# Performance work log

Measured on AMD Instinct MI355X. Metric: run time of the kernel, lower is better.

## Reference

```python
import jax, jax.numpy as jnp
import numpy as np

B, C, H, W = 4, 256, 64, 64
D = C // 8  # qk projection dim = 32


def setup_inputs() -> dict:
    key = jax.random.key(0)
    ks = jax.random.split(key, 10)
    s = 1.0 / np.sqrt(C)
    return {
        "semantic_map": jax.random.normal(ks[0], (B, C, H, W), jnp.float32),
        "structural_map": jax.random.normal(ks[1], (B, C, H, W), jnp.float32),
        "Wq": jax.random.normal(ks[2], (D, C), jnp.float32) * s,
        "bq": jax.random.normal(ks[3], (D,), jnp.float32) * 0.01,
        "Wk": jax.random.normal(ks[4], (D, C), jnp.float32) * s,
        "bk": jax.random.normal(ks[5], (D,), jnp.float32) * 0.01,
        "Wv": jax.random.normal(ks[6], (C, C), jnp.float32) * s,
        "bv": jax.random.normal(ks[7], (C,), jnp.float32) * 0.01,
        "gamma": jnp.zeros((1,), jnp.float32) + 0.5,  # nonzero so the attention path matters
    }


def reference(semantic_map, structural_map, Wq, bq, Wk, bk, Wv, bv, gamma):
    b, c, h, w = semantic_map.shape
    n = h * w
    # 1x1 convs == per-pixel linear projections
    q = jnp.einsum("bchw,dc->bdhw", semantic_map, Wq) + bq[None, :, None, None]
    k = jnp.einsum("bchw,dc->bdhw", structural_map, Wk) + bk[None, :, None, None]
    v = jnp.einsum("bchw,oc->bohw", structural_map, Wv) + bv[None, :, None, None]
    q = q.reshape(b, -1, n).transpose(0, 2, 1)  # (B, HW, D)
    k = k.reshape(b, -1, n)                     # (B, D, HW)
    v = v.reshape(b, c, n)                      # (B, C, HW)
    energy = jnp.einsum("bid,bdj->bij", q, k)   # (B, HW, HW)
    attention = jax.nn.softmax(energy, axis=-1)
    # out[b,c,i] = sum_j v[b,c,j] * attention[b,i,j]
    out = jnp.einsum("bcj,bij->bci", v, attention).reshape(b, c, h, w)
    return gamma * out + semantic_map
```

## Files before the change

kernel.cpp:

```cpp
#include <hip/hip_runtime.h>

#define B_   4
#define C_   256
#define N_   4096
#define D_   32
#define CP   264

typedef _Float16 half8  __attribute__((ext_vector_type(8)));
typedef _Float16 half4v __attribute__((ext_vector_type(4)));
typedef _Float16 half2v __attribute__((ext_vector_type(2)));
typedef float    f32x4  __attribute__((ext_vector_type(4)));

__global__ __launch_bounds__(256) void wcvt_kernel(
    const float* __restrict__ Wq, const float* __restrict__ Wk,
    const float* __restrict__ Wv, _Float16* __restrict__ Wh)
{
    const int idx = blockIdx.x * 256 + threadIdx.x;
    const int kk  = idx & 31;
    const int row = (idx >> 5) & 15;
    const int kc  = (idx >> 9) & 7;
    const int t   = idx >> 12;
    const int c   = kc*32 + kk;
    float v;
    if (t < 2)      v = Wq[(t*16 + row)*C_ + c];
    else if (t < 4) v = Wk[((t-2)*16 + row)*C_ + c];
    else            v = Wv[((t-4)*16 + row)*C_ + c];
    Wh[idx] = (_Float16)v;
}

__global__ __launch_bounds__(512, 4) void proj_kernel(
    const float* __restrict__ sem, const float* __restrict__ str,
    const _Float16* __restrict__ Wh,
    const float* __restrict__ bq, const float* __restrict__ bk,
    const float* __restrict__ bv,
    _Float16* __restrict__ Qh, _Float16* __restrict__ Kh, _Float16* __restrict__ Vh2)
{
    __shared__ __align__(16) _Float16 smem[2 * 64 * CP];
    _Float16* s_x = smem;
    _Float16* s_s = smem + 64 * CP;

    const int bid = blockIdx.x;
    const int nt6 = bid & 63;
    const int b   = bid >> 6;
    const int n0  = nt6 * 64;
    const int tid = threadIdx.x;
    const int w    = tid >> 6;
    const int lane = tid & 63;
    const int quad = lane >> 4;
    const int l15  = lane & 15;

    const int cnt = (w < 4) ? 3 : 2;
    const int t0  = (w < 4) ? w*3 : 12 + (w-4)*2;

    f32x4 acc[3][4];
    #pragma unroll
    for (int i = 0; i < 3; ++i)
        #pragma unroll
        for (int j = 0; j < 4; ++j) { acc[i][j][0]=0.f; acc[i][j][1]=0.f; acc[i][j][2]=0.f; acc[i][j][3]=0.f; }

    const size_t xbase = (size_t)b * C_ * N_;

    #pragma unroll
    for (int r = 0; r < 4; ++r) {
        const int slot = r*512 + tid;
        const int nq = slot & 15;
        const int cp = slot >> 4;
        const float* p0 = str + xbase + (size_t)(2*cp) * N_ + n0 + nq*4;
        const float4 a4 = *(const float4*)p0;
        const float4 b4 = *(const float4*)(p0 + N_);
        #pragma unroll
        for (int t = 0; t < 4; ++t) {
            half2v hp; hp[0] = (_Float16)a4[t]; hp[1] = (_Float16)b4[t];
            *(half2v*)(s_x + (nq*4 + t)*CP + 2*cp) = hp;
        }
        const float* p1 = sem + xbase + (size_t)(2*cp) * N_ + n0 + nq*4;
        const float4 c4 = *(const float4*)p1;
        const float4 d4 = *(const float4*)(p1 + N_);
        #pragma unroll
        for (int t = 0; t < 4; ++t) {
            half2v hp; hp[0] = (_Float16)c4[t]; hp[1] = (_Float16)d4[t];
            *(half2v*)(s_s + (nq*4 + t)*CP + 2*cp) = hp;
        }
    }
    __syncthreads();

    auto afload = [&](half8 (&af)[3], int kc) {
        #pragma unroll
        for (int mi = 0; mi < 3; ++mi)
            if (mi < cnt)
                af[mi] = *(const half8*)(Wh + ((size_t)(((t0+mi)*8 + kc)*16 + l15))*32 + quad*8);
    };
    auto bload = [&](half8 (&bfr)[4], half8 (&sfr)[4], int kc) {
        #pragma unroll
        for (int nt = 0; nt < 4; ++nt)
            bfr[nt] = *(const half8*)(s_x + (nt*16 + l15)*CP + kc*32 + quad*8);
        if (w == 0) {
            #pragma unroll
            for (int nt = 0; nt < 4; ++nt)
                sfr[nt] = *(const half8*)(s_s + (nt*16 + l15)*CP + kc*32 + quad*8);
        }
    };
    auto domfma = [&](const half8 (&af)[3], const half8 (&bfr)[4], const half8 (&sfr)[4]) {
        #pragma unroll
        for (int mi = 0; mi < 3; ++mi) {
            if (mi >= cnt) break;
            const bool useS = (t0 + mi) < 2;
            #pragma unroll
            for (int nt = 0; nt < 4; ++nt)
                acc[mi][nt] = __builtin_amdgcn_mfma_f32_16x16x32_f16(
                                  af[mi], useS ? sfr[nt] : bfr[nt], acc[mi][nt], 0, 0, 0);
        }
    };

    half8 afA[3], afB[3];
    afload(afA, 0);
    #pragma unroll 1
    for (int kc2 = 0; kc2 < 4; ++kc2) {
        const int kc = kc2*2;
        half8 bfr[4], sfr[4];
        bload(bfr, sfr, kc);
        afload(afB, kc+1);
        domfma(afA, bfr, sfr);
        half8 bfr2[4], sfr2[4];
        bload(bfr2, sfr2, kc+1);
        if (kc2 < 3) afload(afA, kc+2);
        domfma(afB, bfr2, sfr2);
    }

    #pragma unroll
    for (int mi = 0; mi < 3; ++mi) {
        if (mi >= cnt) break;
        const int t = t0 + mi;
        if (t < 4) {
            const bool isq = (t < 2);
            const int  tt  = isq ? t : (t - 2);
            f32x4 b4 = *(const f32x4*)((isq ? bq : bk) + tt*16 + quad*4);
            _Float16* dst = isq ? Qh : Kh;
            const int dc  = tt*2 + (quad >> 1);
            const int off = (quad & 1) * 4;
            #pragma unroll
            for (int nt = 0; nt < 4; ++nt) {
                const int n = n0 + nt*16 + l15;
                f32x4 a = acc[mi][nt];
                half4v hq;
                hq[0]=(_Float16)(a[0]+b4[0]); hq[1]=(_Float16)(a[1]+b4[1]);
                hq[2]=(_Float16)(a[2]+b4[2]); hq[3]=(_Float16)(a[3]+b4[3]);
                *(half4v*)(dst + ((size_t)(b*4 + dc) * N_ + n) * 8 + off) = hq;
            }
        }
    }
    __syncthreads();

    #pragma unroll
    for (int mi = 0; mi < 3; ++mi) {
        if (mi >= cnt) break;
        const int t = t0 + mi;
        if (t >= 4) {
            const int ctg = t - 4;
            f32x4 b4 = *(const f32x4*)(bv + ctg*16 + quad*4);
            _Float16* sv = smem + (w*3 + mi)*1024;
            #pragma unroll
            for (int nt = 0; nt < 4; ++nt) {
                const int js = nt & 1;
                const int hb = nt >> 1;
                f32x4 a = acc[mi][nt];
                #pragma unroll
                for (int r = 0; r < 4; ++r)
                    sv[hb*512 + ((l15>>2)*16 + quad*4 + r)*8 + js*4 + (l15&3)]
                        = (_Float16)(a[r] + b4[r]);
            }
        }
    }
    {
        _Float16* vb = Vh2 + (size_t)b * (size_t)N_ * C_;
        const int jc2_0 = n0 >> 5;
        #pragma unroll
        for (int mi = 0; mi < 3; ++mi) {
            if (mi >= cnt) break;
            const int t = t0 + mi;
            if (t >= 4) {
                const int ctg = t - 4;
                const _Float16* sv = smem + (w*3 + mi)*1024;
                #pragma unroll
                for (int hb = 0; hb < 2; ++hb) {
                    half8 vv = *(const half8*)(&sv[hb*512 + lane*8]);
                    *(half8*)(vb + (size_t)(jc2_0 + hb)*8192 + (size_t)ctg*512 + lane*8) = vv;
                }
            }
        }
    }
}

__global__ __launch_bounds__(256, 2) void flash_kernel(
    const _Float16* __restrict__ Qh, const _Float16* __restrict__ Kh,
    const _Float16* __restrict__ Vh2, const float* __restrict__ sem,
    const float* __restrict__ gma, float* __restrict__ out)
{
    __shared__ float s_mp[4*32];
    __shared__ float s_lp[4*32];
    __shared__ __align__(16) float s_red[4][64][32];

    const int bid = blockIdx.x;
    const int xcd = bid & 7;
    const int b   = xcd >> 1;
    const int i0  = ((xcd & 1)*64 + (bid >> 3)) * 32;
    const int tid = threadIdx.x;
    const int w    = tid >> 6;
    const int lane = tid & 63;
    const int quad = lane >> 4;
    const int l15  = lane & 15;
    const int wc   = w & 1;
    const int wj   = w >> 1;

    const _Float16* qk_base = Qh + (size_t)(b*4 + quad) * N_ * 8;
    const half8 qf0 = *(const half8*)(qk_base + (size_t)(i0 + l15) * 8);
    const half8 qf1 = *(const half8*)(qk_base + (size_t)(i0 + 16 + l15) * 8);

    const _Float16* klane = Kh + ((size_t)(b*4 + quad) * N_ + l15) * 8;
    const _Float16* vl    = Vh2 + (size_t)b * (size_t)N_ * C_
                            + (size_t)(wc*8) * 512 + (size_t)lane * 8;

    float mx0 = -3e38f, mx1 = -3e38f;
    {
        half8 kp[4], kn[4];
        auto kl4 = [&](half8 (&kf)[4], int j0) {
            #pragma unroll
            for (int js = 0; js < 4; ++js)
                kf[js] = *(const half8*)(klane + (size_t)(j0 + js*16) * 8);
        };
        auto p0step = [&](const half8 (&kf)[4], half8 (&kfn)[4], int j0, bool more) {
            if (more) kl4(kfn, j0 + 64);
            #pragma unroll
            for (int js = 0; js < 4; ++js) {
                f32x4 z; z[0]=0.f; z[1]=0.f; z[2]=0.f; z[3]=0.f;
                f32x4 s0 = __builtin_amdgcn_mfma_f32_16x16x32_f16(kf[js], qf0, z, 0, 0, 0);
                f32x4 s1 = __builtin_amdgcn_mfma_f32_16x16x32_f16(kf[js], qf1, z, 0, 0, 0);
                #pragma unroll
                for (int r = 0; r < 4; ++r) { mx0 = fmaxf(mx0, s0[r]); mx1 = fmaxf(mx1, s1[r]); }
            }
        };
        kl4(kp, w*1024);
        #pragma unroll 1
        for (int it2 = 0; it2 < 8; ++it2) {
            const int j0 = w*1024 + it2*128;
            p0step(kp, kn, j0, true);
            p0step(kn, kp, j0 + 64, it2 < 7);
        }
    }
    mx0 = fmaxf(mx0, __shfl_xor(mx0, 16)); mx0 = fmaxf(mx0, __shfl_xor(mx0, 32));
    mx1 = fmaxf(mx1, __shfl_xor(mx1, 16)); mx1 = fmaxf(mx1, __shfl_xor(mx1, 32));
    if (lane < 32) s_mp[w*32 + lane] = (lane < 16) ? mx0 : mx1;
    __syncthreads();
    float mf0 = -3e38f, mf1 = -3e38f;
    #pragma unroll
    for (int ww = 0; ww < 4; ++ww) {
        mf0 = fmaxf(mf0, s_mp[ww*32 + l15]);
        mf1 = fmaxf(mf1, s_mp[ww*32 + 16 + l15]);
    }

    f32x4 acc[8][2];
    #pragma unroll
    for (int ct = 0; ct < 8; ++ct)
        #pragma unroll
        for (int f = 0; f < 2; ++f) { acc[ct][f][0]=0.f; acc[ct][f][1]=0.f; acc[ct][f][2]=0.f; acc[ct][f][3]=0.f; }
    float l0 = 0.f, l1 = 0.f;

    half8 kA[2], kB[2], vA[8], vB[8];

    auto kl2 = [&](half8 (&kf)[2], int j0) {
        kf[0] = *(const half8*)(klane + (size_t)j0 * 8);
        kf[1] = *(const half8*)(klane + (size_t)(j0 + 16) * 8);
    };
    auto vl8 = [&](half8 (&vf)[8], int j0) {
        const _Float16* p = vl + (size_t)(j0 >> 5) * 8192;
        #pragma unroll
        for (int ct = 0; ct < 8; ++ct)
            vf[ct] = *(const half8*)(p + ct*512);
    };
    auto mkp = [](const f32x4& s, float mf, float& lacc) -> half4v {
        float e0 = __expf(s[0]-mf), e1 = __expf(s[1]-mf);
        float e2 = __expf(s[2]-mf), e3 = __expf(s[3]-mf);
        lacc += (e0+e1)+(e2+e3);
        half2v p01 = __builtin_bit_cast(half2v, __builtin_amdgcn_cvt_pkrtz(e0, e1));
        half2v p23 = __builtin_bit_cast(half2v, __builtin_amdgcn_cvt_pkrtz(e2, e3));
        return __builtin_shufflevector(p01, p23, 0, 1, 2, 3);
    };

    auto step = [&](const half8 (&kf)[2], const half8 (&vf)[8],
                    half8 (&kfn)[2], half8 (&vfn)[8], int j0, bool more) {
        f32x4 z; z[0]=0.f; z[1]=0.f; z[2]=0.f; z[3]=0.f;
        f32x4 sf0[2], sf1[2];
        #pragma unroll
        for (int js = 0; js < 2; ++js) {
            sf0[js] = __builtin_amdgcn_mfma_f32_16x16x32_f16(kf[js], qf0, z, 0, 0, 0);
            sf1[js] = __builtin_amdgcn_mfma_f32_16x16x32_f16(kf[js], qf1, z, 0, 0, 0);
        }
        if (more) {
            kl2(kfn, j0 + 32);
            vl8(vfn, j0 + 32);
        }
        half4v pa0 = mkp(sf0[0], mf0, l0);
        half4v pb0 = mkp(sf0[1], mf0, l0);
        half4v pa1 = mkp(sf1[0], mf1, l1);
        half4v pb1 = mkp(sf1[1], mf1, l1);
        half8 pcat0 = __builtin_shufflevector(pa0, pb0, 0, 1, 2, 3, 4, 5, 6, 7);
        half8 pcat1 = __builtin_shufflevector(pa1, pb1, 0, 1, 2, 3, 4, 5, 6, 7);
        __builtin_amdgcn_s_setprio(1);
        #pragma unroll
        for (int ct = 0; ct < 8; ++ct) {
            acc[ct][0] = __builtin_amdgcn_mfma_f32_16x16x32_f16(vf[ct], pcat0, acc[ct][0], 0, 0, 0);
            acc[ct][1] = __builtin_amdgcn_mfma_f32_16x16x32_f16(vf[ct], pcat1, acc[ct][1], 0, 0, 0);
        }
        __builtin_amdgcn_s_setprio(0);
    };

    const int jb = wj * 2048;
    kl2(kA, jb);
    vl8(vA, jb);
    #pragma unroll 1
    for (int s2 = 0; s2 < 32; ++s2) {
        const int j0 = jb + s2*64;
        step(kA, vA, kB, vB, j0, true);
        step(kB, vB, kA, vA, j0 + 32, s2 < 31);
    }

    l0 += __shfl_xor(l0, 16); l0 += __shfl_xor(l0, 32);
    l1 += __shfl_xor(l1, 16); l1 += __shfl_xor(l1, 32);
    if (lane < 32) s_lp[w*32 + lane] = (lane < 16) ? l0 : l1;

    const int kx = (lane & 7) << 2;
    if (wj == 0) {
        #pragma unroll
        for (int t2 = 0; t2 < 4; ++t2) {
            *(f32x4*)&s_red[w][lane][(t2*8)     ^ kx] = acc[4 + t2][0];
            *(f32x4*)&s_red[w][lane][(t2*8 + 4) ^ kx] = acc[4 + t2][1];
        }
    } else {
        #pragma unroll
        for (int t2 = 0; t2 < 4; ++t2) {
            *(f32x4*)&s_red[w][lane][(t2*8)     ^ kx] = acc[t2][0];
            *(f32x4*)&s_red[w][lane][(t2*8 + 4) ^ kx] = acc[t2][1];
        }
    }
    __syncthreads();

    const float lt0 = s_lp[wc*32 + l15]      + s_lp[64 + wc*32 + l15];
    const float lt1 = s_lp[wc*32 + 16 + l15] + s_lp[64 + wc*32 + 16 + l15];
    const float g = gma[0];
    const float sc0 = g / lt0, sc1 = g / lt1;
    const int wp = w ^ 2;

    if (wj == 0) {
        #pragma unroll
        for (int t2 = 0; t2 < 4; ++t2) {
            f32x4 r0 = *(const f32x4*)&s_red[wp][lane][(t2*8)     ^ kx];
            f32x4 r1 = *(const f32x4*)&s_red[wp][lane][(t2*8 + 4) ^ kx];
            r0 += acc[t2][0];
            r1 += acc[t2][1];
            const int cb0 = (wc*8 + t2)*16 + quad*4;
            #pragma unroll
            for (int r4 = 0; r4 < 4; ++r4) {
                const size_t idx = ((size_t)(b*C_ + cb0 + r4)) * N_ + i0 + l15;
                out[idx]      = r0[r4] * sc0 + sem[idx];
                out[idx + 16] = r1[r4] * sc1 + sem[idx + 16];
            }
        }
    } else {
        #pragma unroll
        for (int t2 = 0; t2 < 4; ++t2) {
            f32x4 r0 = *(const f32x4*)&s_red[wp][lane][(t2*8)     ^ kx];
            f32x4 r1 = *(const f32x4*)&s_red[wp][lane][(t2*8 + 4) ^ kx];
            r0 += acc[4 + t2][0];
            r1 += acc[4 + t2][1];
            const int cb0 = (wc*8 + 4 + t2)*16 + quad*4;
            #pragma unroll
            for (int r4 = 0; r4 < 4; ++r4) {
                const size_t idx = ((size_t)(b*C_ + cb0 + r4)) * N_ + i0 + l15;
                out[idx]      = r0[r4] * sc0 + sem[idx];
                out[idx + 16] = r1[r4] * sc1 + sem[idx + 16];
            }
        }
    }
}

extern "C" void kernel_launch(void* const* d_in, const int* in_sizes, int n_in,
                              void* d_out, int out_size, void* d_ws, size_t ws_size,
                              hipStream_t stream) {
    const float* sem = (const float*)d_in[0];
    const float* str = (const float*)d_in[1];
    const float* Wq  = (const float*)d_in[2];
    const float* bq  = (const float*)d_in[3];
    const float* Wk  = (const float*)d_in[4];
    const float* bk  = (const float*)d_in[5];
    const float* Wv  = (const float*)d_in[6];
    const float* bv  = (const float*)d_in[7];
    const float* gma = (const float*)d_in[8];
    float* out = (float*)d_out;

    _Float16* Qh  = (_Float16*)d_ws;
    _Float16* Kh  = Qh + (size_t)B_*N_*D_;
    _Float16* Vh2 = Kh + (size_t)B_*N_*D_;
    _Float16* Wh  = Vh2 + (size_t)B_*C_*N_;

    hipLaunchKernelGGL(wcvt_kernel, dim3(320), dim3(256), 0, stream, Wq, Wk, Wv, Wh);
    hipLaunchKernelGGL(proj_kernel, dim3(B_*(N_/64)), dim3(512), 0, stream,
                       sem, str, Wh, bq, bk, bv, Qh, Kh, Vh2);
    hipLaunchKernelGGL(flash_kernel, dim3(B_*(N_/32)), dim3(256), 0, stream,
                       Qh, Kh, Vh2, sem, gma, out);
}
```

Measured before the change: 160.0 us.

## Software-pipeline QK^T and PV MFMAs across iterations in attention loop

Restructures the attention inner loop so the QK^T scores and exp for the next 32-key block are computed while the PV MFMAs for the current block run, with the probabilities carried in registers across steps. A prologue computes the first block's probabilities, and K loads are issued two blocks ahead. The launch bound for proj_kernel drops its minimum blocks per CU from 4 to 2, which lets it use more registers but may lower occupancy. The goal is to hide exp/convert latency behind matrix work, at the cost of higher register pressure.

After: 163.1 us. About the same (+1.9%).

```diff
diff --git a/kernel.cpp b/kernel.cpp
--- a/kernel.cpp
+++ b/kernel.cpp
@@ -28,7 +28,7 @@
     Wh[idx] = (_Float16)v;
 }
 
-__global__ __launch_bounds__(512, 4) void proj_kernel(
+__global__ __launch_bounds__(512, 2) void proj_kernel(
     const float* __restrict__ sem, const float* __restrict__ str,
     const _Float16* __restrict__ Wh,
     const float* __restrict__ bq, const float* __restrict__ bk,
@@ -265,7 +265,8 @@
         for (int f = 0; f < 2; ++f) { acc[ct][f][0]=0.f; acc[ct][f][1]=0.f; acc[ct][f][2]=0.f; acc[ct][f][3]=0.f; }
     float l0 = 0.f, l1 = 0.f;
 
-    half8 kA[2], kB[2], vA[8], vB[8];
+    half8  kA[2], kB[2], vA[8], vB[8];
+    half4v p0a, p0b, p1a, p1b;
 
     auto kl2 = [&](half8 (&kf)[2], int j0) {
         kf[0] = *(const half8*)(klane + (size_t)j0 * 8);
@@ -286,42 +287,55 @@
         return __builtin_shufflevector(p01, p23, 0, 1, 2, 3);
     };
 
-    auto step = [&](const half8 (&kf)[2], const half8 (&vf)[8],
-                    half8 (&kfn)[2], half8 (&vfn)[8], int j0, bool more) {
+    const int jb   = wj * 2048;
+    const int jend = jb + 2048;
+
+    kl2(kA, jb);
+    vl8(vA, jb);
+    kl2(kB, jb + 32);
+    {
+        f32x4 z; z[0]=0.f; z[1]=0.f; z[2]=0.f; z[3]=0.f;
+        f32x4 s00 = __builtin_amdgcn_mfma_f32_16x16x32_f16(kA[0], qf0, z, 0, 0, 0);
+        f32x4 s01 = __builtin_amdgcn_mfma_f32_16x16x32_f16(kA[1], qf0, z, 0, 0, 0);
+        f32x4 s10 = __builtin_amdgcn_mfma_f32_16x16x32_f16(kA[0], qf1, z, 0, 0, 0);
+        f32x4 s11 = __builtin_amdgcn_mfma_f32_16x16x32_f16(kA[1], qf1, z, 0, 0, 0);
+        p0a = mkp(s00, mf0, l0); p0b = mkp(s01, mf0, l0);
+        p1a = mkp(s10, mf1, l1); p1b = mkp(s11, mf1, l1);
+    }
+
+    auto pipe = [&](const half8 (&kN)[2], const half8 (&vC)[8],
+                    half8 (&kL)[2], half8 (&vL)[8], int j0) {
+        const bool doQK = (j0 + 32) < jend;
         f32x4 z; z[0]=0.f; z[1]=0.f; z[2]=0.f; z[3]=0.f;
         f32x4 sf0[2], sf1[2];
-        #pragma unroll
-        for (int js = 0; js < 2; ++js) {
-            sf0[js] = __builtin_amdgcn_mfma_f32_16x16x32_f16(kf[js], qf0, z, 0, 0, 0);
-            sf1[js] = __builtin_amdgcn_mfma_f32_16x16x32_f16(kf[js], qf1, z, 0, 0, 0);
-        }
-        if (more) {
-            kl2(kfn, j0 + 32);
-            vl8(vfn, j0 + 32);
-        }
-        half4v pa0 = mkp(sf0[0], mf0, l0);
-        half4v pb0 = mkp(sf0[1], mf0, l0);
-        half4v pa1 = mkp(sf1[0], mf1, l1);
-        half4v pb1 = mkp(sf1[1], mf1, l1);
-        half8 pcat0 = __builtin_shufflevector(pa0, pb0, 0, 1, 2, 3, 4, 5, 6, 7);
-        half8 pcat1 = __builtin_shufflevector(pa1, pb1, 0, 1, 2, 3, 4, 5, 6, 7);
+        if (doQK) {
+            sf0[0] = __builtin_amdgcn_mfma_f32_16x16x32_f16(kN[0], qf0, z, 0, 0, 0);
+            sf0[1] = __builtin_amdgcn_mfma_f32_16x16x32_f16(kN[1], qf0, z, 0, 0, 0);
+            sf1[0] = __builtin_amdgcn_mfma_f32_16x16x32_f16(kN[0], qf1, z, 0, 0, 0);
+            sf1[1] = __builtin_amdgcn_mfma_f32_16x16x32_f16(kN[1], qf1, z, 0, 0, 0);
+        }
+        if (j0 + 64 < jend) kl2(kL, j0 + 64);
+        if (j0 + 32 < jend) vl8(vL, j0 + 32);
+        half8 pc0 = __builtin_shufflevector(p0a, p0b, 0, 1, 2, 3, 4, 5, 6, 7);
+        half8 pc1 = __builtin_shufflevector(p1a, p1b, 0, 1, 2, 3, 4, 5, 6, 7);
         __builtin_amdgcn_s_setprio(1);
         #pragma unroll
         for (int ct = 0; ct < 8; ++ct) {
-            acc[ct][0] = __builtin_amdgcn_mfma_f32_16x16x32_f16(vf[ct], pcat0, acc[ct][0], 0, 0, 0);
-            acc[ct][1] = __builtin_amdgcn_mfma_f32_16x16x32_f16(vf[ct], pcat1, acc[ct][1], 0, 0, 0);
+            acc[ct][0] = __builtin_amdgcn_mfma_f32_16x16x32_f16(vC[ct], pc0, acc[ct][0], 0, 0, 0);
+            acc[ct][1] = __builtin_amdgcn_mfma_f32_16x16x32_f16(vC[ct], pc1, acc[ct][1], 0, 0, 0);
         }
         __builtin_amdgcn_s_setprio(0);
-    };
-
-    const int jb = wj * 2048;
-    kl2(kA, jb);
-    vl8(vA, jb);
+        if (doQK) {
+            p0a = mkp(sf0[0], mf0, l0); p0b = mkp(sf0[1], mf0, l0);
+            p1a = mkp(sf1[0], mf1, l1); p1b = mkp(sf1[1], mf1, l1);
+        }
+    };
+
     #pragma unroll 1
     for (int s2 = 0; s2 < 32; ++s2) {
         const int j0 = jb + s2*64;
-        step(kA, vA, kB, vB, j0, true);
-        step(kB, vB, kA, vA, j0 + 32, s2 < 31);
+        pipe(kB, vA, kA, vB, j0);
+        pipe(kA, vB, kB, vA, j0 + 32);
     }
 
     l0 += __shfl_xor(l0, 16); l0 += __shfl_xor(l0, 32);
```

## Split flash attention key range across eight waves with two-stage LDS reduction

Applied to the files above, without the earlier changes.

The flash kernel goes from 4 to 8 waves per block. Each pair of waves now sweeps a quarter of the key/value sequence instead of half, which halves the per-wave serial loop and adds more waves to hide latency. The partial accumulators are combined through a two-stage shared-memory reduction with extra barriers, and the shared buffer doubles. The proj kernel's launch-bounds occupancy hint is also relaxed from 4 to 2, which may give it more registers. Risks are higher LDS use and register pressure limiting residency, plus reduction overhead.

Result: slower. 545.7 us (+241.0%).

```diff
diff --git a/kernel.cpp b/kernel.cpp
--- a/kernel.cpp
+++ b/kernel.cpp
@@ -28,7 +28,7 @@
     Wh[idx] = (_Float16)v;
 }
 
-__global__ __launch_bounds__(512, 4) void proj_kernel(
+__global__ __launch_bounds__(512, 2) void proj_kernel(
     const float* __restrict__ sem, const float* __restrict__ str,
     const _Float16* __restrict__ Wh,
     const float* __restrict__ bq, const float* __restrict__ bk,
@@ -191,14 +191,14 @@
     }
 }
 
-__global__ __launch_bounds__(256, 2) void flash_kernel(
+__global__ __launch_bounds__(512, 4) void flash_kernel(
     const _Float16* __restrict__ Qh, const _Float16* __restrict__ Kh,
     const _Float16* __restrict__ Vh2, const float* __restrict__ sem,
     const float* __restrict__ gma, float* __restrict__ out)
 {
-    __shared__ float s_mp[4*32];
-    __shared__ float s_lp[4*32];
-    __shared__ __align__(16) float s_red[4][64][32];
+    __shared__ float s_mp[8*32];
+    __shared__ float s_lp[8*32];
+    __shared__ __align__(16) float s_red[4][64][64];
 
     const int bid = blockIdx.x;
     const int xcd = bid & 7;
@@ -239,12 +239,12 @@
                 for (int r = 0; r < 4; ++r) { mx0 = fmaxf(mx0, s0[r]); mx1 = fmaxf(mx1, s1[r]); }
             }
         };
-        kl4(kp, w*1024);
+        kl4(kp, w*512);
         #pragma unroll 1
-        for (int it2 = 0; it2 < 8; ++it2) {
-            const int j0 = w*1024 + it2*128;
+        for (int it2 = 0; it2 < 4; ++it2) {
+            const int j0 = w*512 + it2*128;
             p0step(kp, kn, j0, true);
-            p0step(kn, kp, j0 + 64, it2 < 7);
+            p0step(kn, kp, j0 + 64, it2 < 3);
         }
     }
     mx0 = fmaxf(mx0, __shfl_xor(mx0, 16)); mx0 = fmaxf(mx0, __shfl_xor(mx0, 32));
@@ -253,7 +253,7 @@
     __syncthreads();
     float mf0 = -3e38f, mf1 = -3e38f;
     #pragma unroll
-    for (int ww = 0; ww < 4; ++ww) {
+    for (int ww = 0; ww < 8; ++ww) {
         mf0 = fmaxf(mf0, s_mp[ww*32 + l15]);
         mf1 = fmaxf(mf1, s_mp[ww*32 + 16 + l15]);
     }
@@ -314,14 +314,14 @@
         __builtin_amdgcn_s_setprio(0);
     };
 
-    const int jb = wj * 2048;
+    const int jb = wj * 1024;
     kl2(kA, jb);
     vl8(vA, jb);
     #pragma unroll 1
-    for (int s2 = 0; s2 < 32; ++s2) {
+    for (int s2 = 0; s2 < 16; ++s2) {
         const int j0 = jb + s2*64;
         step(kA, vA, kB, vB, j0, true);
-        step(kB, vB, kA, vA, j0 + 32, s2 < 31);
+        step(kB, vB, kA, vA, j0 + 32, s2 < 15);
     }
 
     l0 += __shfl_xor(l0, 16); l0 += __shfl_xor(l0, 32);
@@ -329,13 +329,31 @@
     if (lane < 32) s_lp[w*32 + lane] = (lane < 16) ? l0 : l1;
 
     const int kx = (lane & 7) << 2;
-    if (wj == 0) {
+    if (w >= 4) {
+        #pragma unroll
+        for (int ct = 0; ct < 8; ++ct) {
+            *(f32x4*)&s_red[w - 4][lane][(ct*8)     ^ kx] = acc[ct][0];
+            *(f32x4*)&s_red[w - 4][lane][(ct*8 + 4) ^ kx] = acc[ct][1];
+        }
+    }
+    __syncthreads();
+    if (w < 4) {
+        #pragma unroll
+        for (int ct = 0; ct < 8; ++ct) {
+            f32x4 a0 = *(const f32x4*)&s_red[w][lane][(ct*8)     ^ kx];
+            f32x4 a1 = *(const f32x4*)&s_red[w][lane][(ct*8 + 4) ^ kx];
+            acc[ct][0] += a0;
+            acc[ct][1] += a1;
+        }
+    }
+    __syncthreads();
+    if (w < 2) {
         #pragma unroll
         for (int t2 = 0; t2 < 4; ++t2) {
             *(f32x4*)&s_red[w][lane][(t2*8)     ^ kx] = acc[4 + t2][0];
             *(f32x4*)&s_red[w][lane][(t2*8 + 4) ^ kx] = acc[4 + t2][1];
         }
-    } else {
+    } else if (w < 4) {
         #pragma unroll
         for (int t2 = 0; t2 < 4; ++t2) {
             *(f32x4*)&s_red[w][lane][(t2*8)     ^ kx] = acc[t2][0];
@@ -344,40 +362,46 @@
     }
     __syncthreads();
 
-    const float lt0 = s_lp[wc*32 + l15]      + s_lp[64 + wc*32 + l15];
-    const float lt1 = s_lp[wc*32 + 16 + l15] + s_lp[64 + wc*32 + 16 + l15];
-    const float g = gma[0];
-    const float sc0 = g / lt0, sc1 = g / lt1;
-    const int wp = w ^ 2;
-
-    if (wj == 0) {
-        #pragma unroll
-        for (int t2 = 0; t2 < 4; ++t2) {
-            f32x4 r0 = *(const f32x4*)&s_red[wp][lane][(t2*8)     ^ kx];
-            f32x4 r1 = *(const f32x4*)&s_red[wp][lane][(t2*8 + 4) ^ kx];
-            r0 += acc[t2][0];
-            r1 += acc[t2][1];
-            const int cb0 = (wc*8 + t2)*16 + quad*4;
-            #pragma unroll
-            for (int r4 = 0; r4 < 4; ++r4) {
-                const size_t idx = ((size_t)(b*C_ + cb0 + r4)) * N_ + i0 + l15;
-                out[idx]      = r0[r4] * sc0 + sem[idx];
-                out[idx + 16] = r1[r4] * sc1 + sem[idx + 16];
-            }
-        }
-    } else {
-        #pragma unroll
-        for (int t2 = 0; t2 < 4; ++t2) {
-            f32x4 r0 = *(const f32x4*)&s_red[wp][lane][(t2*8)     ^ kx];
-            f32x4 r1 = *(const f32x4*)&s_red[wp][lane][(t2*8 + 4) ^ kx];
-            r0 += acc[4 + t2][0];
-            r1 += acc[4 + t2][1];
-            const int cb0 = (wc*8 + 4 + t2)*16 + quad*4;
-            #pragma unroll
-            for (int r4 = 0; r4 < 4; ++r4) {
-                const size_t idx = ((size_t)(b*C_ + cb0 + r4)) * N_ + i0 + l15;
-                out[idx]      = r0[r4] * sc0 + sem[idx];
-                out[idx + 16] = r1[r4] * sc1 + sem[idx + 16];
+    if (w < 4) {
+        const int mywc = w & 1;
+        const float lt0 = s_lp[(mywc)*32 + l15]      + s_lp[(mywc+2)*32 + l15]
+                        + s_lp[(mywc+4)*32 + l15]    + s_lp[(mywc+6)*32 + l15];
+        const float lt1 = s_lp[(mywc)*32 + 16 + l15] + s_lp[(mywc+2)*32 + 16 + l15]
+                        + s_lp[(mywc+4)*32 + 16 + l15] + s_lp[(mywc+6)*32 + 16 + l15];
+        const float g = gma[0];
+        const float sc0 = g / lt0, sc1 = g / lt1;
+
+        if (w < 2) {
+            #pragma unroll
+            for (int t2 = 0; t2 < 4; ++t2) {
+                f32x4 r0 = acc[t2][0];
+                f32x4 r1 = acc[t2][1];
+                f32x4 o0 = *(const f32x4*)&s_red[w + 2][lane][(t2*8)     ^ kx];
+                f32x4 o1 = *(const f32x4*)&s_red[w + 2][lane][(t2*8 + 4) ^ kx];
+                r0 += o0; r1 += o1;
+                const int cb0 = (mywc*8 + t2)*16 + quad*4;
+                #pragma unroll
+                for (int r4 = 0; r4 < 4; ++r4) {
+                    const size_t idx = ((size_t)(b*C_ + cb0 + r4)) * N_ + i0 + l15;
+                    out[idx]      = r0[r4] * sc0 + sem[idx];
+                    out[idx + 16] = r1[r4] * sc1 + sem[idx + 16];
+                }
+            }
+        } else {
+            #pragma unroll
+            for (int t2 = 0; t2 < 4; ++t2) {
+                f32x4 r0 = acc[4 + t2][0];
+                f32x4 r1 = acc[4 + t2][1];
+                f32x4 o0 = *(const f32x4*)&s_red[w - 2][lane][(t2*8)     ^ kx];
+                f32x4 o1 = *(const f32x4*)&s_red[w - 2][lane][(t2*8 + 4) ^ kx];
+                r0 += o0; r1 += o1;
+                const int cb0 = (mywc*8 + 4 + t2)*16 + quad*4;
+                #pragma unroll
+                for (int r4 = 0; r4 < 4; ++r4) {
+                    const size_t idx = ((size_t)(b*C_ + cb0 + r4)) * N_ + i0 + l15;
+                    out[idx]      = r0[r4] * sc0 + sem[idx];
+                    out[idx + 16] = r1[r4] * sc1 + sem[idx + 16];
+                }
             }
         }
     }
@@ -405,6 +429,6 @@
     hipLaunchKernelGGL(wcvt_kernel, dim3(320), dim3(256), 0, stream, Wq, Wk, Wv, Wh);
     hipLaunchKernelGGL(proj_kernel, dim3(B_*(N_/64)), dim3(512), 0, stream,
                        sem, str, Wh, bq, bk, bv, Qh, Kh, Vh2);
-    hipLaunchKernelGGL(flash_kernel, dim3(B_*(N_/32)), dim3(256), 0, stream,
+    hipLaunchKernelGGL(flash_kernel, dim3(B_*(N_/32)), dim3(512), 0, stream,
                        Qh, Kh, Vh2, sem, gma, out);
 }
```
